# Performance work log

Hardware: AMD Instinct MI355X
Metric: run time of the kernel (lower is better)

Reference implementation:

```python
import jax, jax.numpy as jnp
import numpy as np

B, H = 16384, 1024
EPS = 1e-5


def setup_inputs() -> dict:
    key = jax.random.key(0)
    ks = jax.random.split(key, 12)
    inp = {
        "t": 0,
        "h": jax.random.normal(ks[0], (B, H), jnp.float32),
        "e": jax.random.normal(ks[1], (B, H), jnp.float32),
        # LiquidNeuron params
        "W_rec": jax.random.normal(ks[2], (H, H), jnp.float32) * 0.1,
        "bias": jnp.zeros((H,), jnp.float32),
        "tau": jnp.ones((H,), jnp.float32),
        "decay": jnp.ones((H,), jnp.float32),
        "ln_w": jnp.ones((H,), jnp.float32),
        "ln_b": jnp.zeros((H,), jnp.float32),
        # context_encoder: Linear -> ReLU -> Linear (dropout = identity in eval)
        "ce_w1": jax.random.normal(ks[3], (H, H), jnp.float32) * (1.0 / np.sqrt(H)),
        "ce_b1": jnp.zeros((H,), jnp.float32),
        "ce_w2": jax.random.normal(ks[4], (H, H), jnp.float32) * (1.0 / np.sqrt(H)),
        "ce_b2": jnp.zeros((H,), jnp.float32),
        # param_modulator
        "pm_w": jax.random.normal(ks[5], (H, H), jnp.float32) * (1.0 / np.sqrt(H)),
        "pm_b": jnp.zeros((H,), jnp.float32),
    }
    return inp


def reference(t, h, e, W_rec, bias, tau, decay, ln_w, ln_b,
              ce_w1, ce_b1, ce_w2, ce_b2, pm_w, pm_b):
    # context encoder (eval mode: dropout is identity)
    context = jnp.maximum(h @ ce_w1.T + ce_b1, 0.0) @ ce_w2.T + ce_b2  # [B,H]
    pa = context @ pm_w.T + pm_b  # param_adjustment [B,H]
    # bmm(e[:,None,:], (W_rec*(1+pa)[:,:,None]).T) == (1+pa) * (e @ W_rec.T)
    matmul_result = (1.0 + pa) * (e @ W_rec.T)  # [B,H]
    tau_adjusted = tau * jax.nn.sigmoid(pa)  # [B,H]
    dh_dt = (-decay * h + matmul_result + bias) / tau_adjusted
    # LayerNorm over last dim
    mu = jnp.mean(dh_dt, axis=-1, keepdims=True)
    var = jnp.var(dh_dt, axis=-1, keepdims=True)
    dh_dt = (dh_dt - mu) * jax.lax.rsqrt(var + EPS) * ln_w + ln_b
    return dh_dt
```

## Files before the change

kernel.cpp:

```cpp
#include <hip/hip_runtime.h>
#include <stdint.h>

#define H_DIM 1024
#define B_DIM 16384

typedef unsigned short u16;
typedef short bf16x8 __attribute__((ext_vector_type(8)));
typedef unsigned short ushort8 __attribute__((ext_vector_type(8)));
typedef float f32x4 __attribute__((ext_vector_type(4)));

__device__ __forceinline__ u16 f2bf(float f) {
  union { float f; uint32_t u; } v; v.f = f;
  uint32_t r = v.u + 0x7fffu + ((v.u >> 16) & 1u);
  return (u16)(r >> 16);
}
__device__ __forceinline__ float bf2f(u16 x) {
  union { uint32_t u; float f; } v; v.u = ((uint32_t)x) << 16;
  return v.f;
}

__device__ __forceinline__ bf16x8 cvt8(f32x4 a, f32x4 b) {
  union { uint32_t u[4]; bf16x8 v; } r;
  asm("v_cvt_pk_bf16_f32 %0, %1, %2" : "=v"(r.u[0]) : "v"(a[0]), "v"(a[1]));
  asm("v_cvt_pk_bf16_f32 %0, %1, %2" : "=v"(r.u[1]) : "v"(a[2]), "v"(a[3]));
  asm("v_cvt_pk_bf16_f32 %0, %1, %2" : "=v"(r.u[2]) : "v"(b[0]), "v"(b[1]));
  asm("v_cvt_pk_bf16_f32 %0, %1, %2" : "=v"(r.u[3]) : "v"(b[2]), "v"(b[3]));
  return r.v;
}

#define GLDS16(gsrc, ldst)                                                                 \
  __builtin_amdgcn_global_load_lds((const __attribute__((address_space(1))) void*)(gsrc),  \
                                   (__attribute__((address_space(3))) void*)(ldst), 16, 0, 0)

__device__ __forceinline__ void cvt_region(const float* __restrict__ in, u16* __restrict__ out,
                                           int tid, int nthr, int ngroups) {
  const float4* in4 = (const float4*)in;
  ushort8* out8 = (ushort8*)out;
  for (int gi = tid; gi < ngroups; gi += nthr) {
    float4 a = in4[2 * gi];
    float4 b = in4[2 * gi + 1];
    ushort8 o;
    o[0] = f2bf(a.x); o[1] = f2bf(a.y); o[2] = f2bf(a.z); o[3] = f2bf(a.w);
    o[4] = f2bf(b.x); o[5] = f2bf(b.y); o[6] = f2bf(b.z); o[7] = f2bf(b.w);
    out8[gi] = o;
  }
}

__global__ __launch_bounds__(256) void cvt_w(const float* __restrict__ w1f,
                                             const float* __restrict__ pmwf,
                                             const float* __restrict__ wrecf,
                                             u16* __restrict__ o1, u16* __restrict__ o3,
                                             u16* __restrict__ o4,
                                             const float* __restrict__ tau,
                                             float* __restrict__ rtau) {
  const int b = blockIdx.x;
  const int HH8 = (H_DIM * H_DIM) / 8;
  if (b < 256) {
    cvt_region(w1f, o1, b * 256 + threadIdx.x, 256 * 256, HH8);
  } else if (b < 512) {
    cvt_region(pmwf, o3, (b - 256) * 256 + threadIdx.x, 256 * 256, HH8);
  } else if (b < 768) {
    cvt_region(wrecf, o4, (b - 512) * 256 + threadIdx.x, 256 * 256, HH8);
  } else {
    for (int i = threadIdx.x; i < H_DIM; i += 256) rtau[i] = 1.0f / tau[i];
  }
}

__global__ __launch_bounds__(256) void tr_cvt_w2(const float* __restrict__ in,
                                                 u16* __restrict__ out) {
  __shared__ float tile[64][65];
  const int t = threadIdx.x;
  const int r0 = (blockIdx.x >> 4) * 64;
  const int c0 = (blockIdx.x & 15) * 64;
  const float4* in4 = (const float4*)in;
#pragma unroll
  for (int it = 0; it < 4; ++it) {
    const int idx = it * 256 + t;
    const int r = idx >> 4, c4 = idx & 15;
    float4 v = in4[(size_t)(r0 + r) * 256 + (c0 >> 2) + c4];
    tile[r][c4 * 4 + 0] = v.x; tile[r][c4 * 4 + 1] = v.y;
    tile[r][c4 * 4 + 2] = v.z; tile[r][c4 * 4 + 3] = v.w;
  }
  __syncthreads();
  ushort4* out4 = (ushort4*)out;
#pragma unroll
  for (int it = 0; it < 4; ++it) {
    const int idx = it * 256 + t;
    const int c = idx >> 4, r4 = idx & 15;
    ushort4 o;
    o.x = f2bf(tile[r4 * 4 + 0][c]); o.y = f2bf(tile[r4 * 4 + 1][c]);
    o.z = f2bf(tile[r4 * 4 + 2][c]); o.w = f2bf(tile[r4 * 4 + 3][c]);
    out4[(size_t)(c0 + c) * 256 + (r0 >> 2) + r4] = o;
  }
}

__global__ __launch_bounds__(256) void b32_prep(const float* __restrict__ pmw,
                                                const float* __restrict__ ceb2,
                                                const float* __restrict__ pmb,
                                                float* __restrict__ b32) {
  const int i = blockIdx.x * 256 + threadIdx.x;
  const float4* w4 = (const float4*)(pmw + (size_t)i * H_DIM);
  const float4* b4 = (const float4*)ceb2;
  float acc = pmb[i];
  for (int k = 0; k < 256; ++k) {
    float4 w = w4[k], b = b4[k];
    acc += w.x * b.x + w.y * b.y + w.z * b.z + w.w * b.w;
  }
  b32[i] = acc;
}

__global__ __launch_bounds__(256) void w32_gemm(const u16* __restrict__ A,
                                                const u16* __restrict__ Wt,
                                                u16* __restrict__ C) {
  const int t = threadIdx.x;
  const int wv = t >> 6, l = t & 63;
  const int l15 = l & 15, lg = l >> 4;
  const int m0 = (blockIdx.x >> 4) * 64 + (wv >> 1) * 32;
  const int n0 = (blockIdx.x & 15) * 64 + (wv & 1) * 32;

  const u16* ap0 = A + (size_t)(m0 + l15) * H_DIM + lg * 8;
  const u16* ap1 = ap0 + 16 * H_DIM;
  const u16* bp0 = Wt + (size_t)(n0 + l15) * H_DIM + lg * 8;
  const u16* bp1 = bp0 + 16 * H_DIM;

  f32x4 acc[2][2] = {};
#pragma unroll
  for (int kt = 0; kt < 32; ++kt) {
    bf16x8 aF[2], bF[2];
    aF[0] = *(const bf16x8*)(ap0 + kt * 32);
    aF[1] = *(const bf16x8*)(ap1 + kt * 32);
    bF[0] = *(const bf16x8*)(bp0 + kt * 32);
    bF[1] = *(const bf16x8*)(bp1 + kt * 32);
#pragma unroll
    for (int mi = 0; mi < 2; ++mi)
#pragma unroll
      for (int ni = 0; ni < 2; ++ni)
        acc[mi][ni] =
            __builtin_amdgcn_mfma_f32_16x16x32_bf16(aF[mi], bF[ni], acc[mi][ni], 0, 0, 0);
  }
#pragma unroll
  for (int mi = 0; mi < 2; ++mi)
#pragma unroll
    for (int ni = 0; ni < 2; ++ni) {
      const int col = n0 + ni * 16 + l15;
#pragma unroll
      for (int j = 0; j < 4; ++j) {
        const int row = m0 + mi * 16 + lg * 4 + j;
        C[(size_t)row * H_DIM + col] = f2bf(acc[mi][ni][j]);
      }
    }
}

template <int MODE>
__device__ __forceinline__ void subtile_step(u16* shp, int slot, int slot3, int aoff, int boff,
                                             int wv, const u16*& pA0, const u16*& pA1,
                                             const u16*& pB0, const u16*& pB1,
                                             f32x4 (&acc)[8][4]) {
  const u16* Ab = shp + slot * 16384 + aoff;
  const u16* Bb = shp + slot * 16384 + 8192 + boff;
  bf16x8 aF[8], bF[4];
#pragma unroll
  for (int i = 0; i < 4; ++i) aF[i] = *(const bf16x8*)(Ab + i * 512);
#pragma unroll
  for (int i = 0; i < 4; ++i) bF[i] = *(const bf16x8*)(Bb + i * 512);
#pragma unroll
  for (int i = 4; i < 8; ++i) aF[i] = *(const bf16x8*)(Ab + i * 512);
  if (MODE == 3) {
    u16* da = shp + slot3 * 16384 + wv * 1024;
    GLDS16(pA0, da); GLDS16(pA1, da + 512);
    u16* db = shp + slot3 * 16384 + 8192 + wv * 1024;
    GLDS16(pB0, db); GLDS16(pB1, db + 512);
    pA0 += 32; pA1 += 32; pB0 += 32; pB1 += 32;
  }
  __builtin_amdgcn_s_setprio(1);
#pragma unroll
  for (int mf = 0; mf < 8; ++mf)
#pragma unroll
    for (int nf = 0; nf < 4; ++nf)
      acc[mf][nf] = __builtin_amdgcn_mfma_f32_16x16x32_bf16(aF[mf], bF[nf], acc[mf][nf], 0, 0, 0);
  __builtin_amdgcn_s_setprio(0);
  if (MODE == 3) asm volatile("s_waitcnt vmcnt(8)" ::: "memory");
  if (MODE == 2) asm volatile("s_waitcnt vmcnt(4)" ::: "memory");
  if (MODE == 1) asm volatile("s_waitcnt vmcnt(0)" ::: "memory");
  __builtin_amdgcn_s_barrier();
}

template <bool RELU, bool HASBIAS, typename OUT>
__global__ __launch_bounds__(512, 2) void gemm256(const u16* __restrict__ A,
                                                  const u16* __restrict__ W,
                                                  const float* __restrict__ bias,
                                                  OUT* __restrict__ C) {
  extern __shared__ u16 sh[];
  const int t = threadIdx.x;
  const int wv = t >> 6, l = t & 63;
  const int wm = wv >> 2, wn = wv & 3;
  const int l15 = l & 15, lg = l >> 4;

  const int bid = blockIdx.x;
  const int logical = (bid & 7) * 32 + (bid >> 3);
  const int m0 = (logical >> 2) * 256;
  const int n0 = (logical & 3) * 256;

  const int koff = (lg ^ ((l15 >> 1) & 3)) * 8;
  const int aoff = (wm * 128 + l15) * 32 + koff;
  const int boff = (wn * 64 + l15) * 32 + koff;

  const int rowst = wv * 32 + (l >> 2);
  const int ksl = ((l & 3) ^ ((l >> 3) & 3)) * 8;
  const u16* pA0 = A + (size_t)(m0 + rowst) * H_DIM + ksl;
  const u16* pA1 = pA0 + 16 * H_DIM;
  const u16* pB0 = W + (size_t)(n0 + rowst) * H_DIM + ksl;
  const u16* pB1 = pB0 + 16 * H_DIM;

  f32x4 acc[8][4] = {};

#pragma unroll
  for (int s = 0; s < 3; ++s) {
    u16* da = sh + s * 16384 + wv * 1024;
    GLDS16(pA0, da); GLDS16(pA1, da + 512);
    u16* db = sh + s * 16384 + 8192 + wv * 1024;
    GLDS16(pB0, db); GLDS16(pB1, db + 512);
    pA0 += 32; pA1 += 32; pB0 += 32; pB1 += 32;
  }
  asm volatile("s_waitcnt vmcnt(8)" ::: "memory");
  __builtin_amdgcn_s_barrier();

  for (int s = 0; s < 29; ++s)
    subtile_step<3>(sh, s & 3, (s + 3) & 3, aoff, boff, wv, pA0, pA1, pB0, pB1, acc);
  subtile_step<2>(sh, 1, 0, aoff, boff, wv, pA0, pA1, pB0, pB1, acc);
  subtile_step<1>(sh, 2, 0, aoff, boff, wv, pA0, pA1, pB0, pB1, acc);
  subtile_step<0>(sh, 3, 0, aoff, boff, wv, pA0, pA1, pB0, pB1, acc);

  float bv[4];
#pragma unroll
  for (int nf = 0; nf < 4; ++nf)
    bv[nf] = HASBIAS ? bias[n0 + wn * 64 + nf * 16 + l15] : 0.0f;
#pragma unroll
  for (int mf = 0; mf < 8; ++mf) {
#pragma unroll
    for (int nf = 0; nf < 4; ++nf) {
      const int col = n0 + wn * 64 + nf * 16 + l15;
#pragma unroll
      for (int j = 0; j < 4; ++j) {
        const int row = m0 + wm * 128 + mf * 16 + lg * 4 + j;
        float v = acc[mf][nf][j] + bv[nf];
        if (RELU) v = fmaxf(v, 0.0f);
        if constexpr (sizeof(OUT) == 2)
          C[(size_t)row * H_DIM + col] = (OUT)f2bf(v);
        else
          C[(size_t)row * H_DIM + col] = v;
      }
    }
  }
}

template <int SLOT, int SLOT2, int MODE>
__device__ __forceinline__ void sub_f32(u16* sh, int aoff0, int aoff1, int boff, int wv,
                                        const float*& gA, const u16*& pB0, const u16*& pB1,
                                        f32x4 (&acc)[8][4]) {
  const char* Ab = (const char*)sh + SLOT * 32768;
  const u16* Bb = sh + 49152 + SLOT * 8192 + boff;
  bf16x8 aF[8], bF[4];
#pragma unroll
  for (int mf = 0; mf < 8; ++mf) {
    f32x4 lo = *(const f32x4*)(Ab + aoff0 + mf * 2048);
    f32x4 hi = *(const f32x4*)(Ab + aoff1 + mf * 2048);
    aF[mf] = cvt8(lo, hi);
  }
#pragma unroll
  for (int i = 0; i < 4; ++i) bF[i] = *(const bf16x8*)(Bb + i * 512);
  if (MODE == 2) {
#pragma unroll
    for (int i = 0; i < 4; ++i)
      GLDS16(gA + i * 8 * H_DIM, sh + SLOT2 * 16384 + (wv * 32 + i * 8) * 64);
    gA += 32;
    u16* db = sh + 49152 + SLOT2 * 8192 + wv * 1024;
    GLDS16(pB0, db); GLDS16(pB1, db + 512);
    pB0 += 32; pB1 += 32;
  }
  __builtin_amdgcn_s_setprio(1);
#pragma unroll
  for (int mf = 0; mf < 8; ++mf)
#pragma unroll
    for (int nf = 0; nf < 4; ++nf)
      acc[mf][nf] = __builtin_amdgcn_mfma_f32_16x16x32_bf16(aF[mf], bF[nf], acc[mf][nf], 0, 0, 0);
  __builtin_amdgcn_s_setprio(0);
  if (MODE == 2) asm volatile("s_waitcnt vmcnt(6)" ::: "memory");
  if (MODE == 1) asm volatile("s_waitcnt vmcnt(0)" ::: "memory");
  __builtin_amdgcn_s_barrier();
}

template <bool RELU, bool HASBIAS>
__global__ __launch_bounds__(512, 1) void gemm256_f32a(const float* __restrict__ A,
                                                       const u16* __restrict__ W,
                                                       const float* __restrict__ bias,
                                                       u16* __restrict__ C) {
  extern __shared__ u16 sh[];
  const int t = threadIdx.x;
  const int wv = t >> 6, l = t & 63;
  const int wm = wv >> 2, wn = wv & 3;
  const int l15 = l & 15, lg = l >> 4;

  const int bid = blockIdx.x;
  const int logical = (bid & 7) * 32 + (bid >> 3);
  const int m0 = (logical >> 2) * 256;
  const int n0 = (logical & 3) * 256;

  const int arow = (wm * 128 + l15) * 128;
  const int aoff0 = arow + (((lg << 1) | 0) ^ (l15 & 7)) * 16;
  const int aoff1 = arow + (((lg << 1) | 1) ^ (l15 & 7)) * 16;
  const int boff = (wn * 64 + l15) * 32 + (lg ^ ((l15 >> 1) & 3)) * 8;

  const float* gA = A + (size_t)(m0 + wv * 32 + (l >> 3)) * H_DIM + (((l & 7) ^ ((l >> 3) & 7)) << 2);
  const int rowst = wv * 32 + (l >> 2);
  const int ksl = ((l & 3) ^ ((l >> 3) & 3)) * 8;
  const u16* pB0 = W + (size_t)(n0 + rowst) * H_DIM + ksl;
  const u16* pB1 = pB0 + 16 * H_DIM;

  f32x4 acc[8][4] = {};

#pragma unroll
  for (int s = 0; s < 2; ++s) {
#pragma unroll
    for (int i = 0; i < 4; ++i)
      GLDS16(gA + i * 8 * H_DIM, sh + s * 16384 + (wv * 32 + i * 8) * 64);
    gA += 32;
    u16* db = sh + 49152 + s * 8192 + wv * 1024;
    GLDS16(pB0, db); GLDS16(pB1, db + 512);
    pB0 += 32; pB1 += 32;
  }
  asm volatile("s_waitcnt vmcnt(6)" ::: "memory");
  __builtin_amdgcn_s_barrier();

  for (int su = 0; su < 10; ++su) {
    sub_f32<0, 2, 2>(sh, aoff0, aoff1, boff, wv, gA, pB0, pB1, acc);
    sub_f32<1, 0, 2>(sh, aoff0, aoff1, boff, wv, gA, pB0, pB1, acc);
    sub_f32<2, 1, 2>(sh, aoff0, aoff1, boff, wv, gA, pB0, pB1, acc);
  }
  sub_f32<0, 0, 1>(sh, aoff0, aoff1, boff, wv, gA, pB0, pB1, acc);
  sub_f32<1, 0, 0>(sh, aoff0, aoff1, boff, wv, gA, pB0, pB1, acc);

  float bv[4];
#pragma unroll
  for (int nf = 0; nf < 4; ++nf)
    bv[nf] = HASBIAS ? bias[n0 + wn * 64 + nf * 16 + l15] : 0.0f;
#pragma unroll
  for (int mf = 0; mf < 8; ++mf) {
#pragma unroll
    for (int nf = 0; nf < 4; ++nf) {
      const int col = n0 + wn * 64 + nf * 16 + l15;
#pragma unroll
      for (int j = 0; j < 4; ++j) {
        const int row = m0 + wm * 128 + mf * 16 + lg * 4 + j;
        float v = acc[mf][nf][j] + bv[nf];
        if (RELU) v = fmaxf(v, 0.0f);
        C[(size_t)row * H_DIM + col] = f2bf(v);
      }
    }
  }
}

__global__ __launch_bounds__(256) void liquid_ln(const float* __restrict__ h,
                                                 const u16* __restrict__ pa,
                                                 const u16* __restrict__ ev,
                                                 const float* __restrict__ bias,
                                                 const float* __restrict__ rtau,
                                                 const float* __restrict__ decay,
                                                 const float* __restrict__ lnw,
                                                 const float* __restrict__ lnb,
                                                 float* __restrict__ out) {
  const int wv = threadIdx.x >> 6, l = threadIdx.x & 63;
  const int row = blockIdx.x * 4 + wv;
  const size_t rb = (size_t)row * H_DIM;

  float d[16];
  float s = 0.f, ss = 0.f;
#pragma unroll
  for (int c = 0; c < 2; ++c) {
    const int col = c * 512 + l * 8;
    float h8[8], b8[8], r8[8], dc8[8];
    *(float4*)h8 = *(const float4*)(h + rb + col);
    *(float4*)(h8 + 4) = *(const float4*)(h + rb + col + 4);
    *(float4*)b8 = *(const float4*)(bias + col);
    *(float4*)(b8 + 4) = *(const float4*)(bias + col + 4);
    *(float4*)r8 = *(const float4*)(rtau + col);
    *(float4*)(r8 + 4) = *(const float4*)(rtau + col + 4);
    *(float4*)dc8 = *(const float4*)(decay + col);
    *(float4*)(dc8 + 4) = *(const float4*)(decay + col + 4);
    ushort8 pv = *(const ushort8*)(pa + rb + col);
    ushort8 evv = *(const ushort8*)(ev + rb + col);
#pragma unroll
    for (int j = 0; j < 8; ++j) {
      const float p = bf2f(pv[j]);
      const float e = bf2f(evv[j]);
      const float num = fmaf(-dc8[j], h8[j], fmaf(1.0f + p, e, b8[j]));
      const float val = num * (1.0f + __expf(-p)) * r8[j];
      d[c * 8 + j] = val;
      s += val;
      ss += val * val;
    }
  }
#pragma unroll
  for (int off = 32; off; off >>= 1) {
    s += __shfl_xor(s, off);
    ss += __shfl_xor(ss, off);
  }
  const float mu = s * (1.0f / H_DIM);
  const float var = ss * (1.0f / H_DIM) - mu * mu;
  const float rstd = rsqrtf(var + 1e-5f);

#pragma unroll
  for (int c = 0; c < 2; ++c) {
    const int col = c * 512 + l * 8;
    float w8[8], lb8[8], o[8];
    *(float4*)w8 = *(const float4*)(lnw + col);
    *(float4*)(w8 + 4) = *(const float4*)(lnw + col + 4);
    *(float4*)lb8 = *(const float4*)(lnb + col);
    *(float4*)(lb8 + 4) = *(const float4*)(lnb + col + 4);
#pragma unroll
    for (int j = 0; j < 8; ++j) o[j] = fmaf((d[c * 8 + j] - mu) * rstd, w8[j], lb8[j]);
    *(float4*)(out + rb + col) = *(float4*)o;
    *(float4*)(out + rb + col + 4) = *(float4*)(o + 4);
  }
}

extern "C" void kernel_launch(void* const* d_in, const int* in_sizes, int n_in,
                              void* d_out, int out_size, void* d_ws, size_t ws_size,
                              hipStream_t stream) {
  const float* h = (const float*)d_in[1];
  const float* e = (const float*)d_in[2];
  const float* Wrec = (const float*)d_in[3];
  const float* bias = (const float*)d_in[4];
  const float* tau = (const float*)d_in[5];
  const float* decay = (const float*)d_in[6];
  const float* lnw = (const float*)d_in[7];
  const float* lnb = (const float*)d_in[8];
  const float* ce_w1 = (const float*)d_in[9];
  const float* ce_b1 = (const float*)d_in[10];
  const float* ce_w2 = (const float*)d_in[11];
  const float* ce_b2 = (const float*)d_in[12];
  const float* pm_w = (const float*)d_in[13];
  const float* pm_b = (const float*)d_in[14];
  float* out = (float*)d_out;

  char* ws = (char*)d_ws;
  const size_t MB = 1024 * 1024;
  u16* w1b = (u16*)(ws + 0 * MB);
  u16* w2t = (u16*)(ws + 2 * MB);
  u16* w3b = (u16*)(ws + 4 * MB);
  u16* w4b = (u16*)(ws + 6 * MB);
  u16* W32b = (u16*)(ws + 8 * MB);
  float* rtau = (float*)(ws + 10 * MB);
  float* b32 = (float*)(ws + 10 * MB + 8192);
  u16* t1 = (u16*)(ws + 12 * MB);
  u16* pab = (u16*)(ws + 44 * MB);
  u16* evb = (u16*)(ws + 76 * MB);

  cvt_w<<<769, 256, 0, stream>>>(ce_w1, pm_w, Wrec, w1b, w3b, w4b, tau, rtau);
  tr_cvt_w2<<<256, 256, 0, stream>>>(ce_w2, w2t);
  b32_prep<<<4, 256, 0, stream>>>(pm_w, ce_b2, pm_b, b32);
  w32_gemm<<<256, 256, 0, stream>>>(w3b, w2t, W32b);

  const int LDS_BF16 = 131072;
  const int LDS_F32 = 147456;
  hipFuncSetAttribute((const void*)gemm256_f32a<true, true>,
                      hipFuncAttributeMaxDynamicSharedMemorySize, LDS_F32);
  hipFuncSetAttribute((const void*)gemm256_f32a<false, false>,
                      hipFuncAttributeMaxDynamicSharedMemorySize, LDS_F32);
  hipFuncSetAttribute((const void*)gemm256<false, true, u16>,
                      hipFuncAttributeMaxDynamicSharedMemorySize, LDS_BF16);

  const int NWG = (B_DIM / 256) * (H_DIM / 256);
  gemm256_f32a<true, true><<<NWG, 512, LDS_F32, stream>>>(h, w1b, ce_b1, t1);
  gemm256<false, true, u16><<<NWG, 512, LDS_BF16, stream>>>(t1, W32b, b32, pab);
  gemm256_f32a<false, false><<<NWG, 512, LDS_F32, stream>>>(e, w4b, nullptr, evb);

  liquid_ln<<<B_DIM / 4, 256, 0, stream>>>(h, pab, evb, bias, rtau, decay, lnw, lnb, out);
}
```

Before: 220.8 us.

## Convert fp32 A tiles to bf16 in registers before LDS in f32-input GEMMs

The fp32-input GEMMs no longer copy raw fp32 A tiles into LDS with direct global-to-LDS loads and convert them after each LDS read. Each thread now loads fp32 A into registers two k-steps ahead, converts to bf16 once, and writes bf16 into a 4-slot LDS ring that shares slots with B, so fragments are read with plain bf16 loads. This halves A's LDS footprint and bandwidth and drops the redundant per-wave conversion. In exchange it adds register pressure, a register-staged load path, and an extra lgkmcnt wait before every barrier.

```diff
diff --git a/kernel.cpp b/kernel.cpp
--- a/kernel.cpp
+++ b/kernel.cpp
@@ -19,12 +19,12 @@
   return v.f;
 }
 
-__device__ __forceinline__ bf16x8 cvt8(f32x4 a, f32x4 b) {
+__device__ __forceinline__ bf16x8 cvt8(float4 a, float4 b) {
   union { uint32_t u[4]; bf16x8 v; } r;
-  asm("v_cvt_pk_bf16_f32 %0, %1, %2" : "=v"(r.u[0]) : "v"(a[0]), "v"(a[1]));
-  asm("v_cvt_pk_bf16_f32 %0, %1, %2" : "=v"(r.u[1]) : "v"(a[2]), "v"(a[3]));
-  asm("v_cvt_pk_bf16_f32 %0, %1, %2" : "=v"(r.u[2]) : "v"(b[0]), "v"(b[1]));
-  asm("v_cvt_pk_bf16_f32 %0, %1, %2" : "=v"(r.u[3]) : "v"(b[2]), "v"(b[3]));
+  asm("v_cvt_pk_bf16_f32 %0, %1, %2" : "=v"(r.u[0]) : "v"(a.x), "v"(a.y));
+  asm("v_cvt_pk_bf16_f32 %0, %1, %2" : "=v"(r.u[1]) : "v"(a.z), "v"(a.w));
+  asm("v_cvt_pk_bf16_f32 %0, %1, %2" : "=v"(r.u[2]) : "v"(b.x), "v"(b.y));
+  asm("v_cvt_pk_bf16_f32 %0, %1, %2" : "=v"(r.u[3]) : "v"(b.z), "v"(b.w));
   return r.v;
 }
 
@@ -254,27 +254,34 @@
   }
 }
 
-template <int SLOT, int SLOT2, int MODE>
-__device__ __forceinline__ void sub_f32(u16* sh, int aoff0, int aoff1, int boff, int wv,
-                                        const float*& gA, const u16*& pB0, const u16*& pB1,
-                                        f32x4 (&acc)[8][4]) {
-  const char* Ab = (const char*)sh + SLOT * 32768;
-  const u16* Bb = sh + 49152 + SLOT * 8192 + boff;
+template <int SLOT, int MODE>
+__device__ __forceinline__ void step_f32r(u16* sh, int aoff, int boff, int wv, int dw0,
+                                          const float*& gA0, const float*& gA1,
+                                          const u16*& pB0, const u16*& pB1,
+                                          float4 (&setW)[4], float4 (&setL)[4],
+                                          f32x4 (&acc)[8][4]) {
+  const u16* Ab = sh + SLOT * 16384 + aoff;
+  const u16* Bb = sh + SLOT * 16384 + 8192 + boff;
   bf16x8 aF[8], bF[4];
 #pragma unroll
-  for (int mf = 0; mf < 8; ++mf) {
-    f32x4 lo = *(const f32x4*)(Ab + aoff0 + mf * 2048);
-    f32x4 hi = *(const f32x4*)(Ab + aoff1 + mf * 2048);
-    aF[mf] = cvt8(lo, hi);
-  }
+  for (int i = 0; i < 4; ++i) aF[i] = *(const bf16x8*)(Ab + i * 512);
 #pragma unroll
   for (int i = 0; i < 4; ++i) bF[i] = *(const bf16x8*)(Bb + i * 512);
+#pragma unroll
+  for (int i = 4; i < 8; ++i) aF[i] = *(const bf16x8*)(Ab + i * 512);
+  if (MODE >= 1) {
+    asm volatile("s_waitcnt vmcnt(2)" ::: "memory");
+    u16* wb = sh + ((SLOT + 1) & 3) * 16384;
+    *(bf16x8*)(wb + dw0) = cvt8(setW[0], setW[1]);
+    *(bf16x8*)(wb + dw0 + 4096) = cvt8(setW[2], setW[3]);
+  }
   if (MODE == 2) {
-#pragma unroll
-    for (int i = 0; i < 4; ++i)
-      GLDS16(gA + i * 8 * H_DIM, sh + SLOT2 * 16384 + (wv * 32 + i * 8) * 64);
-    gA += 32;
-    u16* db = sh + 49152 + SLOT2 * 8192 + wv * 1024;
+    setL[0] = *(const float4*)(gA0);
+    setL[1] = *(const float4*)(gA0 + 4);
+    setL[2] = *(const float4*)(gA1);
+    setL[3] = *(const float4*)(gA1 + 4);
+    gA0 += 32; gA1 += 32;
+    u16* db = sh + ((SLOT + 2) & 3) * 16384 + 8192 + wv * 1024;
     GLDS16(pB0, db); GLDS16(pB1, db + 512);
     pB0 += 32; pB1 += 32;
   }
@@ -287,11 +294,12 @@
   __builtin_amdgcn_s_setprio(0);
   if (MODE == 2) asm volatile("s_waitcnt vmcnt(6)" ::: "memory");
   if (MODE == 1) asm volatile("s_waitcnt vmcnt(0)" ::: "memory");
+  asm volatile("s_waitcnt lgkmcnt(0)" ::: "memory");
   __builtin_amdgcn_s_barrier();
 }
 
 template <bool RELU, bool HASBIAS>
-__global__ __launch_bounds__(512, 1) void gemm256_f32a(const float* __restrict__ A,
+__global__ __launch_bounds__(512, 1) void gemm256_f32r(const float* __restrict__ A,
                                                        const u16* __restrict__ W,
                                                        const float* __restrict__ bias,
                                                        u16* __restrict__ C) {
@@ -306,39 +314,53 @@
   const int m0 = (logical >> 2) * 256;
   const int n0 = (logical & 3) * 256;
 
-  const int arow = (wm * 128 + l15) * 128;
-  const int aoff0 = arow + (((lg << 1) | 0) ^ (l15 & 7)) * 16;
-  const int aoff1 = arow + (((lg << 1) | 1) ^ (l15 & 7)) * 16;
-  const int boff = (wn * 64 + l15) * 32 + (lg ^ ((l15 >> 1) & 3)) * 8;
-
-  const float* gA = A + (size_t)(m0 + wv * 32 + (l >> 3)) * H_DIM + (((l & 7) ^ ((l >> 3) & 7)) << 2);
+  const int koff = (lg ^ ((l15 >> 1) & 3)) * 8;
+  const int aoff = (wm * 128 + l15) * 32 + koff;
+  const int boff = (wn * 64 + l15) * 32 + koff;
+
+  const int rbase = t >> 2;
+  const int s4 = t & 3;
+  const int dw0 = rbase * 32 + (s4 ^ ((rbase >> 1) & 3)) * 8;
+  const float* gA0 = A + (size_t)(m0 + rbase) * H_DIM + s4 * 8;
+  const float* gA1 = gA0 + (size_t)128 * H_DIM;
+
   const int rowst = wv * 32 + (l >> 2);
   const int ksl = ((l & 3) ^ ((l >> 3) & 3)) * 8;
   const u16* pB0 = W + (size_t)(n0 + rowst) * H_DIM + ksl;
   const u16* pB1 = pB0 + 16 * H_DIM;
 
   f32x4 acc[8][4] = {};
-
+  float4 sE[4], sO[4];
+
+  sE[0] = *(const float4*)(gA0); sE[1] = *(const float4*)(gA0 + 4);
+  sE[2] = *(const float4*)(gA1); sE[3] = *(const float4*)(gA1 + 4);
+  gA0 += 32; gA1 += 32;
+  sO[0] = *(const float4*)(gA0); sO[1] = *(const float4*)(gA0 + 4);
+  sO[2] = *(const float4*)(gA1); sO[3] = *(const float4*)(gA1 + 4);
+  gA0 += 32; gA1 += 32;
 #pragma unroll
   for (int s = 0; s < 2; ++s) {
-#pragma unroll
-    for (int i = 0; i < 4; ++i)
-      GLDS16(gA + i * 8 * H_DIM, sh + s * 16384 + (wv * 32 + i * 8) * 64);
-    gA += 32;
-    u16* db = sh + 49152 + s * 8192 + wv * 1024;
+    u16* db = sh + s * 16384 + 8192 + wv * 1024;
     GLDS16(pB0, db); GLDS16(pB1, db + 512);
     pB0 += 32; pB1 += 32;
   }
-  asm volatile("s_waitcnt vmcnt(6)" ::: "memory");
+  asm volatile("s_waitcnt vmcnt(4)" ::: "memory");
+  *(bf16x8*)(sh + dw0) = cvt8(sE[0], sE[1]);
+  *(bf16x8*)(sh + dw0 + 4096) = cvt8(sE[2], sE[3]);
+  asm volatile("s_waitcnt vmcnt(2)" ::: "memory");
+  asm volatile("s_waitcnt lgkmcnt(0)" ::: "memory");
   __builtin_amdgcn_s_barrier();
 
-  for (int su = 0; su < 10; ++su) {
-    sub_f32<0, 2, 2>(sh, aoff0, aoff1, boff, wv, gA, pB0, pB1, acc);
-    sub_f32<1, 0, 2>(sh, aoff0, aoff1, boff, wv, gA, pB0, pB1, acc);
-    sub_f32<2, 1, 2>(sh, aoff0, aoff1, boff, wv, gA, pB0, pB1, acc);
-  }
-  sub_f32<0, 0, 1>(sh, aoff0, aoff1, boff, wv, gA, pB0, pB1, acc);
-  sub_f32<1, 0, 0>(sh, aoff0, aoff1, boff, wv, gA, pB0, pB1, acc);
+  for (int su = 0; su < 7; ++su) {
+    step_f32r<0, 2>(sh, aoff, boff, wv, dw0, gA0, gA1, pB0, pB1, sO, sE, acc);
+    step_f32r<1, 2>(sh, aoff, boff, wv, dw0, gA0, gA1, pB0, pB1, sE, sO, acc);
+    step_f32r<2, 2>(sh, aoff, boff, wv, dw0, gA0, gA1, pB0, pB1, sO, sE, acc);
+    step_f32r<3, 2>(sh, aoff, boff, wv, dw0, gA0, gA1, pB0, pB1, sE, sO, acc);
+  }
+  step_f32r<0, 2>(sh, aoff, boff, wv, dw0, gA0, gA1, pB0, pB1, sO, sE, acc);
+  step_f32r<1, 2>(sh, aoff, boff, wv, dw0, gA0, gA1, pB0, pB1, sE, sO, acc);
+  step_f32r<2, 1>(sh, aoff, boff, wv, dw0, gA0, gA1, pB0, pB1, sO, sE, acc);
+  step_f32r<3, 0>(sh, aoff, boff, wv, dw0, gA0, gA1, pB0, pB1, sE, sO, acc);
 
   float bv[4];
 #pragma unroll
@@ -461,19 +483,18 @@
   b32_prep<<<4, 256, 0, stream>>>(pm_w, ce_b2, pm_b, b32);
   w32_gemm<<<256, 256, 0, stream>>>(w3b, w2t, W32b);
 
-  const int LDS_BF16 = 131072;
-  const int LDS_F32 = 147456;
-  hipFuncSetAttribute((const void*)gemm256_f32a<true, true>,
-                      hipFuncAttributeMaxDynamicSharedMemorySize, LDS_F32);
-  hipFuncSetAttribute((const void*)gemm256_f32a<false, false>,
-                      hipFuncAttributeMaxDynamicSharedMemorySize, LDS_F32);
+  const int LDS_BYTES = 131072;
+  hipFuncSetAttribute((const void*)gemm256_f32r<true, true>,
+                      hipFuncAttributeMaxDynamicSharedMemorySize, LDS_BYTES);
+  hipFuncSetAttribute((const void*)gemm256_f32r<false, false>,
+                      hipFuncAttributeMaxDynamicSharedMemorySize, LDS_BYTES);
   hipFuncSetAttribute((const void*)gemm256<false, true, u16>,
-                      hipFuncAttributeMaxDynamicSharedMemorySize, LDS_BF16);
+                      hipFuncAttributeMaxDynamicSharedMemorySize, LDS_BYTES);
 
   const int NWG = (B_DIM / 256) * (H_DIM / 256);
-  gemm256_f32a<true, true><<<NWG, 512, LDS_F32, stream>>>(h, w1b, ce_b1, t1);
-  gemm256<false, true, u16><<<NWG, 512, LDS_BF16, stream>>>(t1, W32b, b32, pab);
-  gemm256_f32a<false, false><<<NWG, 512, LDS_F32, stream>>>(e, w4b, nullptr, evb);
+  gemm256_f32r<true, true><<<NWG, 512, LDS_BYTES, stream>>>(h, w1b, ce_b1, t1);
+  gemm256<false, true, u16><<<NWG, 512, LDS_BYTES, stream>>>(t1, W32b, b32, pab);
+  gemm256_f32r<false, false><<<NWG, 512, LDS_BYTES, stream>>>(e, w4b, nullptr, evb);
 
   liquid_ln<<<B_DIM / 4, 256, 0, stream>>>(h, pab, evb, bias, rtau, decay, lnw, lnb, out);
 }
```

After: 222.6 us. Within noise of the previous version (+0.8%).

## Restructure fp32-A GEMM LDS layout and pipeline; merge weight-prep kernels

Applied to the files above, without the earlier changes.

The fp32-input GEMM now stores each K-step's A tile as two 16-float halves with a new swizzle. A and B share one 48KB slot, and the loop runs a uniform 3-slot ring that issues the next global-to-LDS loads before the LDS fragment reads. The bf16 GEMM step likewise issues its prefetch before the fragment reads. The weight-conversion kernel uses half as many blocks, each batching 8 float4 loads, and the w2 transpose and bias-fold kernels are merged into one launch. The aims are to cut launch overhead, hide global load latency behind MFMA work, and reduce LDS bank conflicts; the new swizzle and wait counts risk correctness or conflict regressions.

```diff
diff --git a/kernel.cpp b/kernel.cpp
--- a/kernel.cpp
+++ b/kernel.cpp
@@ -18,8 +18,12 @@
   union { uint32_t u; float f; } v; v.u = ((uint32_t)x) << 16;
   return v.f;
 }
-
-__device__ __forceinline__ bf16x8 cvt8(f32x4 a, f32x4 b) {
+__device__ __forceinline__ ushort4 cvt4(float4 a) {
+  ushort4 o;
+  o.x = f2bf(a.x); o.y = f2bf(a.y); o.z = f2bf(a.z); o.w = f2bf(a.w);
+  return o;
+}
+__device__ __forceinline__ bf16x8 cvt8f(f32x4 a, f32x4 b) {
   union { uint32_t u[4]; bf16x8 v; } r;
   asm("v_cvt_pk_bf16_f32 %0, %1, %2" : "=v"(r.u[0]) : "v"(a[0]), "v"(a[1]));
   asm("v_cvt_pk_bf16_f32 %0, %1, %2" : "=v"(r.u[1]) : "v"(a[2]), "v"(a[3]));
@@ -31,20 +35,6 @@
 #define GLDS16(gsrc, ldst)                                                                 \
   __builtin_amdgcn_global_load_lds((const __attribute__((address_space(1))) void*)(gsrc),  \
                                    (__attribute__((address_space(3))) void*)(ldst), 16, 0, 0)
-
-__device__ __forceinline__ void cvt_region(const float* __restrict__ in, u16* __restrict__ out,
-                                           int tid, int nthr, int ngroups) {
-  const float4* in4 = (const float4*)in;
-  ushort8* out8 = (ushort8*)out;
-  for (int gi = tid; gi < ngroups; gi += nthr) {
-    float4 a = in4[2 * gi];
-    float4 b = in4[2 * gi + 1];
-    ushort8 o;
-    o[0] = f2bf(a.x); o[1] = f2bf(a.y); o[2] = f2bf(a.z); o[3] = f2bf(a.w);
-    o[4] = f2bf(b.x); o[5] = f2bf(b.y); o[6] = f2bf(b.z); o[7] = f2bf(b.w);
-    out8[gi] = o;
-  }
-}
 
 __global__ __launch_bounds__(256) void cvt_w(const float* __restrict__ w1f,
                                              const float* __restrict__ pmwf,
@@ -54,22 +44,60 @@
                                              const float* __restrict__ tau,
                                              float* __restrict__ rtau) {
   const int b = blockIdx.x;
-  const int HH8 = (H_DIM * H_DIM) / 8;
-  if (b < 256) {
-    cvt_region(w1f, o1, b * 256 + threadIdx.x, 256 * 256, HH8);
-  } else if (b < 512) {
-    cvt_region(pmwf, o3, (b - 256) * 256 + threadIdx.x, 256 * 256, HH8);
-  } else if (b < 768) {
-    cvt_region(wrecf, o4, (b - 512) * 256 + threadIdx.x, 256 * 256, HH8);
+  const int t = threadIdx.x;
+  const float* in;
+  u16* out;
+  int chunk;
+  if (b < 128) {
+    in = w1f; out = o1; chunk = b;
+  } else if (b < 256) {
+    in = pmwf; out = o3; chunk = b - 128;
+  } else if (b < 384) {
+    in = wrecf; out = o4; chunk = b - 256;
   } else {
-    for (int i = threadIdx.x; i < H_DIM; i += 256) rtau[i] = 1.0f / tau[i];
-  }
-}
-
-__global__ __launch_bounds__(256) void tr_cvt_w2(const float* __restrict__ in,
-                                                 u16* __restrict__ out) {
+    for (int i = t; i < H_DIM; i += 256) rtau[i] = 1.0f / tau[i];
+    return;
+  }
+  const float4* in4 = (const float4*)in + (size_t)chunk * 2048;
+  ushort8* out8 = (ushort8*)out + (size_t)chunk * 1024;
+  float4 v[8];
+#pragma unroll
+  for (int g = 0; g < 4; ++g) {
+    const int oi = g * 256 + t;
+    v[2 * g] = in4[2 * oi];
+    v[2 * g + 1] = in4[2 * oi + 1];
+  }
+#pragma unroll
+  for (int g = 0; g < 4; ++g) {
+    const int oi = g * 256 + t;
+    ushort4 lo = cvt4(v[2 * g]), hi = cvt4(v[2 * g + 1]);
+    ushort8 o;
+    o[0] = lo.x; o[1] = lo.y; o[2] = lo.z; o[3] = lo.w;
+    o[4] = hi.x; o[5] = hi.y; o[6] = hi.z; o[7] = hi.w;
+    out8[oi] = o;
+  }
+}
+
+__global__ __launch_bounds__(256) void tr_cvt_w2_b32(const float* __restrict__ in,
+                                                     u16* __restrict__ out,
+                                                     const float* __restrict__ pmw,
+                                                     const float* __restrict__ ceb2,
+                                                     const float* __restrict__ pmb,
+                                                     float* __restrict__ b32) {
+  const int t = threadIdx.x;
+  if (blockIdx.x >= 256) {
+    const int i = (blockIdx.x - 256) * 256 + t;
+    const float4* w4 = (const float4*)(pmw + (size_t)i * H_DIM);
+    const float4* b4 = (const float4*)ceb2;
+    float acc = pmb[i];
+    for (int k = 0; k < 256; ++k) {
+      float4 w = w4[k], b = b4[k];
+      acc += w.x * b.x + w.y * b.y + w.z * b.z + w.w * b.w;
+    }
+    b32[i] = acc;
+    return;
+  }
   __shared__ float tile[64][65];
-  const int t = threadIdx.x;
   const int r0 = (blockIdx.x >> 4) * 64;
   const int c0 = (blockIdx.x & 15) * 64;
   const float4* in4 = (const float4*)in;
@@ -92,21 +120,6 @@
     o.z = f2bf(tile[r4 * 4 + 2][c]); o.w = f2bf(tile[r4 * 4 + 3][c]);
     out4[(size_t)(c0 + c) * 256 + (r0 >> 2) + r4] = o;
   }
-}
-
-__global__ __launch_bounds__(256) void b32_prep(const float* __restrict__ pmw,
-                                                const float* __restrict__ ceb2,
-                                                const float* __restrict__ pmb,
-                                                float* __restrict__ b32) {
-  const int i = blockIdx.x * 256 + threadIdx.x;
-  const float4* w4 = (const float4*)(pmw + (size_t)i * H_DIM);
-  const float4* b4 = (const float4*)ceb2;
-  float acc = pmb[i];
-  for (int k = 0; k < 256; ++k) {
-    float4 w = w4[k], b = b4[k];
-    acc += w.x * b.x + w.y * b.y + w.z * b.z + w.w * b.w;
-  }
-  b32[i] = acc;
 }
 
 __global__ __launch_bounds__(256) void w32_gemm(const u16* __restrict__ A,
@@ -156,15 +169,6 @@
                                              int wv, const u16*& pA0, const u16*& pA1,
                                              const u16*& pB0, const u16*& pB1,
                                              f32x4 (&acc)[8][4]) {
-  const u16* Ab = shp + slot * 16384 + aoff;
-  const u16* Bb = shp + slot * 16384 + 8192 + boff;
-  bf16x8 aF[8], bF[4];
-#pragma unroll
-  for (int i = 0; i < 4; ++i) aF[i] = *(const bf16x8*)(Ab + i * 512);
-#pragma unroll
-  for (int i = 0; i < 4; ++i) bF[i] = *(const bf16x8*)(Bb + i * 512);
-#pragma unroll
-  for (int i = 4; i < 8; ++i) aF[i] = *(const bf16x8*)(Ab + i * 512);
   if (MODE == 3) {
     u16* da = shp + slot3 * 16384 + wv * 1024;
     GLDS16(pA0, da); GLDS16(pA1, da + 512);
@@ -172,6 +176,15 @@
     GLDS16(pB0, db); GLDS16(pB1, db + 512);
     pA0 += 32; pA1 += 32; pB0 += 32; pB1 += 32;
   }
+  const u16* Ab = shp + slot * 16384 + aoff;
+  const u16* Bb = shp + slot * 16384 + 8192 + boff;
+  bf16x8 aF[8], bF[4];
+#pragma unroll
+  for (int i = 0; i < 4; ++i) aF[i] = *(const bf16x8*)(Ab + i * 512);
+#pragma unroll
+  for (int i = 0; i < 4; ++i) bF[i] = *(const bf16x8*)(Bb + i * 512);
+#pragma unroll
+  for (int i = 4; i < 8; ++i) aF[i] = *(const bf16x8*)(Ab + i * 512);
   __builtin_amdgcn_s_setprio(1);
 #pragma unroll
   for (int mf = 0; mf < 8; ++mf)
@@ -254,30 +267,34 @@
   }
 }
 
-template <int SLOT, int SLOT2, int MODE>
-__device__ __forceinline__ void sub_f32(u16* sh, int aoff0, int aoff1, int boff, int wv,
+template <int MODE>
+__device__ __forceinline__ void sub_f32(char* shc, int slot, int slot2, int areg, int as0,
+                                        int as1, int arow, int boffB, int wv,
                                         const float*& gA, const u16*& pB0, const u16*& pB1,
                                         f32x4 (&acc)[8][4]) {
-  const char* Ab = (const char*)sh + SLOT * 32768;
-  const u16* Bb = sh + 49152 + SLOT * 8192 + boff;
+  char* sb = shc + slot * 49152;
+  if (MODE == 3) {
+    char* sb2 = shc + slot2 * 49152;
+    GLDS16(gA, sb2 + (wv * 32) * 64);
+    GLDS16(gA + 16 * H_DIM, sb2 + (wv * 32 + 16) * 64);
+    GLDS16(gA + 16, sb2 + 16384 + (wv * 32) * 64);
+    GLDS16(gA + 16 * H_DIM + 16, sb2 + 16384 + (wv * 32 + 16) * 64);
+    gA += 32;
+    char* db = sb2 + 32768 + wv * 2048;
+    GLDS16(pB0, db); GLDS16(pB1, db + 1024);
+    pB0 += 32; pB1 += 32;
+  }
+  const char* Ab = sb + areg;
   bf16x8 aF[8], bF[4];
 #pragma unroll
   for (int mf = 0; mf < 8; ++mf) {
-    f32x4 lo = *(const f32x4*)(Ab + aoff0 + mf * 2048);
-    f32x4 hi = *(const f32x4*)(Ab + aoff1 + mf * 2048);
-    aF[mf] = cvt8(lo, hi);
-  }
+    f32x4 lo = *(const f32x4*)(Ab + arow + mf * 1024 + as0);
+    f32x4 hi = *(const f32x4*)(Ab + arow + mf * 1024 + as1);
+    aF[mf] = cvt8f(lo, hi);
+  }
+  const u16* Bb = (const u16*)(sb + boffB);
 #pragma unroll
   for (int i = 0; i < 4; ++i) bF[i] = *(const bf16x8*)(Bb + i * 512);
-  if (MODE == 2) {
-#pragma unroll
-    for (int i = 0; i < 4; ++i)
-      GLDS16(gA + i * 8 * H_DIM, sh + SLOT2 * 16384 + (wv * 32 + i * 8) * 64);
-    gA += 32;
-    u16* db = sh + 49152 + SLOT2 * 8192 + wv * 1024;
-    GLDS16(pB0, db); GLDS16(pB1, db + 512);
-    pB0 += 32; pB1 += 32;
-  }
   __builtin_amdgcn_s_setprio(1);
 #pragma unroll
   for (int mf = 0; mf < 8; ++mf)
@@ -285,17 +302,17 @@
     for (int nf = 0; nf < 4; ++nf)
       acc[mf][nf] = __builtin_amdgcn_mfma_f32_16x16x32_bf16(aF[mf], bF[nf], acc[mf][nf], 0, 0, 0);
   __builtin_amdgcn_s_setprio(0);
-  if (MODE == 2) asm volatile("s_waitcnt vmcnt(6)" ::: "memory");
+  if (MODE == 3) asm volatile("s_waitcnt vmcnt(6)" ::: "memory");
   if (MODE == 1) asm volatile("s_waitcnt vmcnt(0)" ::: "memory");
   __builtin_amdgcn_s_barrier();
 }
 
 template <bool RELU, bool HASBIAS>
-__global__ __launch_bounds__(512, 1) void gemm256_f32a(const float* __restrict__ A,
-                                                       const u16* __restrict__ W,
-                                                       const float* __restrict__ bias,
-                                                       u16* __restrict__ C) {
-  extern __shared__ u16 sh[];
+__global__ __launch_bounds__(512, 1) void gemm256_f32(const float* __restrict__ A,
+                                                      const u16* __restrict__ W,
+                                                      const float* __restrict__ bias,
+                                                      u16* __restrict__ C) {
+  extern __shared__ char shc[];
   const int t = threadIdx.x;
   const int wv = t >> 6, l = t & 63;
   const int wm = wv >> 2, wn = wv & 3;
@@ -306,12 +323,15 @@
   const int m0 = (logical >> 2) * 256;
   const int n0 = (logical & 3) * 256;
 
-  const int arow = (wm * 128 + l15) * 128;
-  const int aoff0 = arow + (((lg << 1) | 0) ^ (l15 & 7)) * 16;
-  const int aoff1 = arow + (((lg << 1) | 1) ^ (l15 & 7)) * 16;
-  const int boff = (wn * 64 + l15) * 32 + (lg ^ ((l15 >> 1) & 3)) * 8;
-
-  const float* gA = A + (size_t)(m0 + wv * 32 + (l >> 3)) * H_DIM + (((l & 7) ^ ((l >> 3) & 7)) << 2);
+  const int aswz = (l15 >> 1) & 3;
+  const int areg = (lg >> 1) * 16384;
+  const int as0 = (((lg & 1) * 2 + 0) ^ aswz) * 16;
+  const int as1 = (((lg & 1) * 2 + 1) ^ aswz) * 16;
+  const int arow = (wm * 128 + l15) * 64;
+  const int boffB = 32768 + (((wn * 64 + l15) * 32 + (lg ^ aswz) * 8) << 1);
+
+  const float* gA = A + (size_t)(m0 + wv * 32 + (l >> 2)) * H_DIM
+                      + (((l & 3) ^ ((l >> 3) & 3)) << 2);
   const int rowst = wv * 32 + (l >> 2);
   const int ksl = ((l & 3) ^ ((l >> 3) & 3)) * 8;
   const u16* pB0 = W + (size_t)(n0 + rowst) * H_DIM + ksl;
@@ -321,24 +341,23 @@
 
 #pragma unroll
   for (int s = 0; s < 2; ++s) {
-#pragma unroll
-    for (int i = 0; i < 4; ++i)
-      GLDS16(gA + i * 8 * H_DIM, sh + s * 16384 + (wv * 32 + i * 8) * 64);
+    char* sb2 = shc + s * 49152;
+    GLDS16(gA, sb2 + (wv * 32) * 64);
+    GLDS16(gA + 16 * H_DIM, sb2 + (wv * 32 + 16) * 64);
+    GLDS16(gA + 16, sb2 + 16384 + (wv * 32) * 64);
+    GLDS16(gA + 16 * H_DIM + 16, sb2 + 16384 + (wv * 32 + 16) * 64);
     gA += 32;
-    u16* db = sh + 49152 + s * 8192 + wv * 1024;
-    GLDS16(pB0, db); GLDS16(pB1, db + 512);
+    char* db = sb2 + 32768 + wv * 2048;
+    GLDS16(pB0, db); GLDS16(pB1, db + 1024);
     pB0 += 32; pB1 += 32;
   }
   asm volatile("s_waitcnt vmcnt(6)" ::: "memory");
   __builtin_amdgcn_s_barrier();
 
-  for (int su = 0; su < 10; ++su) {
-    sub_f32<0, 2, 2>(sh, aoff0, aoff1, boff, wv, gA, pB0, pB1, acc);
-    sub_f32<1, 0, 2>(sh, aoff0, aoff1, boff, wv, gA, pB0, pB1, acc);
-    sub_f32<2, 1, 2>(sh, aoff0, aoff1, boff, wv, gA, pB0, pB1, acc);
-  }
-  sub_f32<0, 0, 1>(sh, aoff0, aoff1, boff, wv, gA, pB0, pB1, acc);
-  sub_f32<1, 0, 0>(sh, aoff0, aoff1, boff, wv, gA, pB0, pB1, acc);
+  for (int s = 0; s < 30; ++s)
+    sub_f32<3>(shc, s % 3, (s + 2) % 3, areg, as0, as1, arow, boffB, wv, gA, pB0, pB1, acc);
+  sub_f32<1>(shc, 0, 0, areg, as0, as1, arow, boffB, wv, gA, pB0, pB1, acc);
+  sub_f32<0>(shc, 1, 0, areg, as0, as1, arow, boffB, wv, gA, pB0, pB1, acc);
 
   float bv[4];
 #pragma unroll
@@ -456,24 +475,23 @@
   u16* pab = (u16*)(ws + 44 * MB);
   u16* evb = (u16*)(ws + 76 * MB);
 
-  cvt_w<<<769, 256, 0, stream>>>(ce_w1, pm_w, Wrec, w1b, w3b, w4b, tau, rtau);
-  tr_cvt_w2<<<256, 256, 0, stream>>>(ce_w2, w2t);
-  b32_prep<<<4, 256, 0, stream>>>(pm_w, ce_b2, pm_b, b32);
+  cvt_w<<<385, 256, 0, stream>>>(ce_w1, pm_w, Wrec, w1b, w3b, w4b, tau, rtau);
+  tr_cvt_w2_b32<<<260, 256, 0, stream>>>(ce_w2, w2t, pm_w, ce_b2, pm_b, b32);
   w32_gemm<<<256, 256, 0, stream>>>(w3b, w2t, W32b);
 
   const int LDS_BF16 = 131072;
   const int LDS_F32 = 147456;
-  hipFuncSetAttribute((const void*)gemm256_f32a<true, true>,
+  hipFuncSetAttribute((const void*)gemm256_f32<true, true>,
                       hipFuncAttributeMaxDynamicSharedMemorySize, LDS_F32);
-  hipFuncSetAttribute((const void*)gemm256_f32a<false, false>,
+  hipFuncSetAttribute((const void*)gemm256_f32<false, false>,
                       hipFuncAttributeMaxDynamicSharedMemorySize, LDS_F32);
   hipFuncSetAttribute((const void*)gemm256<false, true, u16>,
                       hipFuncAttributeMaxDynamicSharedMemorySize, LDS_BF16);
 
   const int NWG = (B_DIM / 256) * (H_DIM / 256);
-  gemm256_f32a<true, true><<<NWG, 512, LDS_F32, stream>>>(h, w1b, ce_b1, t1);
+  gemm256_f32<true, true><<<NWG, 512, LDS_F32, stream>>>(h, w1b, ce_b1, t1);
   gemm256<false, true, u16><<<NWG, 512, LDS_BF16, stream>>>(t1, W32b, b32, pab);
-  gemm256_f32a<false, false><<<NWG, 512, LDS_F32, stream>>>(e, w4b, nullptr, evb);
+  gemm256_f32<false, false><<<NWG, 512, LDS_F32, stream>>>(e, w4b, nullptr, evb);
 
   liquid_ln<<<B_DIM / 4, 256, 0, stream>>>(h, pab, evb, bias, rtau, decay, lnw, lnb, out);
 }
```

After: 226.2 us. 1.02x slower.
